# Kernel optimization log

Hardware: AMD Instinct MI355X
Metric: run time of the kernel (lower is better)

The kernel has to match this reference:

```python
import jax, jax.numpy as jnp
import numpy as np

H = 256  # GRU hidden size
V = 56   # decoder vocab / fc1 out


def gru_cell(x, h, wih, whh, bih, bhh):
    # PyTorch GRU cell math (gate order: r, z, n)
    gi = x @ wih.T + bih
    gh = h @ whh.T + bhh
    ir, iz, inn = jnp.split(gi, 3, axis=-1)
    hr, hz, hn = jnp.split(gh, 3, axis=-1)
    r = jax.nn.sigmoid(ir + hr)
    z = jax.nn.sigmoid(iz + hz)
    n = jnp.tanh(inn + r * hn)
    return (1.0 - z) * n + z * h


def gru_scan(seq, h0, wih, whh, bih, bhh):
    def step(h, xt):
        h = gru_cell(xt, h, wih, whh, bih, bhh)
        return h, h
    hT, ys = jax.lax.scan(step, h0, seq)
    return ys, hT


def bigru(seq, pf, pb):
    # seq: (S, N, F). Returns (S, N, 2H), final fwd hidden (N,H), final bwd hidden (N,H)
    S, N, _ = seq.shape
    h0 = jnp.zeros((N, H), seq.dtype)
    yf, hf = gru_scan(seq, h0, *pf)
    yb_rev, hb = gru_scan(seq[::-1], h0, *pb)
    return jnp.concatenate([yf, yb_rev[::-1]], axis=-1), hf, hb


def setup_inputs() -> dict:
    key = jax.random.key(0)
    ks = iter(jax.random.split(key, 32))
    s = 0.05
    p = {}
    p["x"] = jax.random.normal(next(ks), (64, 48, 512, 2, 2), dtype=jnp.float32)
    # bi_gru_1: input 192
    for d in ("f", "b"):
        p[f"w_ih_1{d}"] = jax.random.normal(next(ks), (3 * H, 192), jnp.float32) * s
        p[f"w_hh_1{d}"] = jax.random.normal(next(ks), (3 * H, H), jnp.float32) * s
        p[f"b_ih_1{d}"] = jax.random.normal(next(ks), (3 * H,), jnp.float32) * s
        p[f"b_hh_1{d}"] = jax.random.normal(next(ks), (3 * H,), jnp.float32) * s
    # bi_gru_2: input 512
    for d in ("f", "b"):
        p[f"w_ih_2{d}"] = jax.random.normal(next(ks), (3 * H, 2 * H), jnp.float32) * s
        p[f"w_hh_2{d}"] = jax.random.normal(next(ks), (3 * H, H), jnp.float32) * s
        p[f"b_ih_2{d}"] = jax.random.normal(next(ks), (3 * H,), jnp.float32) * s
        p[f"b_hh_2{d}"] = jax.random.normal(next(ks), (3 * H,), jnp.float32) * s
    # decoder GRU: input 56
    p["w_ih_d"] = jax.random.normal(next(ks), (3 * H, V), jnp.float32) * s
    p["w_hh_d"] = jax.random.normal(next(ks), (3 * H, H), jnp.float32) * s
    p["b_ih_d"] = jax.random.normal(next(ks), (3 * H,), jnp.float32) * s
    p["b_hh_d"] = jax.random.normal(next(ks), (3 * H,), jnp.float32) * s
    p["w_fc1"] = jax.random.normal(next(ks), (V, H), jnp.float32) * s
    p["b_fc1"] = jax.random.normal(next(ks), (V,), jnp.float32) * s
    p["w_adj"] = jax.random.normal(next(ks), (H, 2 * H), jnp.float32) * s
    p["b_adj"] = jax.random.normal(next(ks), (H,), jnp.float32) * s
    p["target_length"] = 6
    return p


def reference(x,
              w_ih_1f, w_hh_1f, b_ih_1f, b_hh_1f,
              w_ih_1b, w_hh_1b, b_ih_1b, b_hh_1b,
              w_ih_2f, w_hh_2f, b_ih_2f, b_hh_2f,
              w_ih_2b, w_hh_2b, b_ih_2b, b_hh_2b,
              w_ih_d, w_hh_d, b_ih_d, b_hh_d,
              w_fc1, b_fc1, w_adj, b_adj,
              target_length):
    B, C, T, Hh, Ww = x.shape
    # permute(2,0,1,3,4).contiguous().view(B, T, -1): flat buffer in (T,B,..) order reshaped to (B,T,feat)
    seq = jnp.transpose(x, (2, 0, 1, 3, 4)).reshape(B, T, C * Hh * Ww)
    # GRUs run seq-first: seq dim = B, batch dim = T (faithful to the torch code)
    y1, _, _ = bigru(seq, (w_ih_1f, w_hh_1f, b_ih_1f, b_hh_1f),
                     (w_ih_1b, w_hh_1b, b_ih_1b, b_hh_1b))
    # dropout is identity at inference
    y2, hf, hb = bigru(y1, (w_ih_2f, w_hh_2f, b_ih_2f, b_hh_2f),
                       (w_ih_2b, w_hh_2b, b_ih_2b, b_hh_2b))
    combined = jnp.concatenate([hf, hb], axis=-1)       # (T, 2H)
    dec_h_all = combined @ w_adj.T + b_adj              # (T, H)
    dec_h = dec_h_all[:B]                               # loop over b in range(B) selects first B rows
    inp0 = jnp.zeros((B, V), x.dtype)

    def step(carry, _):
        inp, h = carry
        h = gru_cell(inp, h, w_ih_d, w_hh_d, b_ih_d, b_hh_d)
        out = h @ w_fc1.T + b_fc1
        return (out, h), out

    _, outs = jax.lax.scan(step, (inp0, dec_h), None, length=target_length)
    return jnp.transpose(outs, (1, 0, 2))  # (B, target_length, V)
```

## Files before the change

### kernel.cpp

```cpp
#include <hip/hip_runtime.h>
#include <hip/hip_fp16.h>
#include <stdint.h>


#define HD 256
#define G3 768
#define NSEQ 64
#define NSTEP 64

typedef _Float16 hvec2 __attribute__((ext_vector_type(2)));
typedef _Float16 f16x8 __attribute__((ext_vector_type(8)));
typedef float f32x4 __attribute__((ext_vector_type(4)));

__device__ __forceinline__ float sigmf(float x) {
    return 1.0f / (1.0f + __expf(-x));
}

#if __has_builtin(__builtin_amdgcn_fdot2)
__device__ __forceinline__ float fdot2u(uint32_t w, uint32_t h, float acc) {
    return __builtin_amdgcn_fdot2(__builtin_bit_cast(hvec2, w),
                                  __builtin_bit_cast(hvec2, h), acc, false);
}
#else
__device__ __forceinline__ float fdot2u(uint32_t w, uint32_t h, float acc) {
    const __half2 wv = __builtin_bit_cast(__half2, w);
    const __half2 hv = __builtin_bit_cast(__half2, h);
    acc += __half2float(wv.x) * __half2float(hv.x);
    acc += __half2float(wv.y) * __half2float(hv.y);
    return acc;
}
#endif

__device__ __forceinline__ uint32_t pkh(float a, float b) {
    uint32_t lo = __half_as_ushort(__float2half_rn(a));
    uint32_t hi = __half_as_ushort(__float2half_rn(b));
    return lo | (hi << 16);
}

#define L16(X) X(0) X(1) X(2) X(3) X(4) X(5) X(6) X(7) \
  X(8) X(9) X(10) X(11) X(12) X(13) X(14) X(15)

#define LRES(i) \
    const uint4 wr##i = wbase[(i) * G3]; \
    const uint4 wz##i = wbase[(i) * G3 + 256]; \
    const uint4 wn##i = wbase[(i) * G3 + 512];

#define DRES(i) { \
    const uint4 hp = *(const uint4*)&hb[hoff + 4 * (i)]; \
    ar0 = fdot2u(wr##i.x, hp.x, ar0); ar1 = fdot2u(wr##i.y, hp.y, ar1); \
    ar0 = fdot2u(wr##i.z, hp.z, ar0); ar1 = fdot2u(wr##i.w, hp.w, ar1); \
    az0 = fdot2u(wz##i.x, hp.x, az0); az1 = fdot2u(wz##i.y, hp.y, az1); \
    az0 = fdot2u(wz##i.z, hp.z, az0); az1 = fdot2u(wz##i.w, hp.w, az1); \
    an0 = fdot2u(wn##i.x, hp.x, an0); an1 = fdot2u(wn##i.y, hp.y, an1); \
    an0 = fdot2u(wn##i.z, hp.z, an0); an1 = fdot2u(wn##i.w, hp.w, an1); }

__global__ __launch_bounds__(256) void pack_whhT(
    const float* __restrict__ w0, const float* __restrict__ w1,
    const float* __restrict__ w2, const float* __restrict__ w3,
    const float* __restrict__ w4,
    uint32_t* __restrict__ o0, uint32_t* __restrict__ o1,
    uint32_t* __restrict__ o2, uint32_t* __restrict__ o3,
    uint32_t* __restrict__ o4)
{
    const float* w; uint32_t* o;
    switch (blockIdx.y) {
        case 0: w = w0; o = o0; break;
        case 1: w = w1; o = o1; break;
        case 2: w = w2; o = o2; break;
        case 3: w = w3; o = o3; break;
        default: w = w4; o = o4; break;
    }
    int idx = blockIdx.x * 256 + threadIdx.x;
    int j = idx >> 5, q = idx & 31;
    const float4 fa = *(const float4*)(w + j * HD + 8 * q);
    const float4 fb = *(const float4*)(w + j * HD + 8 * q + 4);
    uint4 r;
    r.x = pkh(fa.x, fa.y);
    r.y = pkh(fa.z, fa.w);
    r.z = pkh(fb.x, fb.y);
    r.w = pkh(fb.z, fb.w);
    ((uint4*)o)[q * G3 + j] = r;
}

__global__ __launch_bounds__(256) void pack_wih(
    const float* __restrict__ s0, const float* __restrict__ s1,
    const float* __restrict__ s2, const float* __restrict__ s3,
    __half* __restrict__ d0, __half* __restrict__ d1,
    __half* __restrict__ d2, __half* __restrict__ d3)
{
    const float* s; __half* d; int sz;
    switch (blockIdx.y) {
        case 0: s = s0; d = d0; sz = 147456; break;
        case 1: s = s1; d = d1; sz = 147456; break;
        case 2: s = s2; d = d2; sz = 393216; break;
        default: s = s3; d = d3; sz = 393216; break;
    }
    int i4 = blockIdx.x * 256 + threadIdx.x;
    if (i4 * 4 >= sz) return;
    const float4 v = *(const float4*)(s + i4 * 4);
    __half2 lo; lo.x = __float2half_rn(v.x); lo.y = __float2half_rn(v.y);
    __half2 hi; hi.x = __float2half_rn(v.z); hi.y = __float2half_rn(v.w);
    *(__half2*)(d + i4 * 4)     = lo;
    *(__half2*)(d + i4 * 4 + 2) = hi;
}

__global__ __launch_bounds__(256) void prep_small(
    const float* __restrict__ wihd,
    const float* __restrict__ wadj,
    const float* __restrict__ wfc1,
    float* __restrict__ wihdT,
    float* __restrict__ wadjT,
    float* __restrict__ wfc1T)
{
    int idx = blockIdx.x * 256 + threadIdx.x;
    if (idx < 43008) {
        int v = idx / G3, j = idx % G3;
        wihdT[idx] = wihd[j * 56 + v];
    } else if (idx < 43008 + 131072) {
        int i2 = idx - 43008;
        int f = i2 / HD, i = i2 % HD;
        wadjT[i2] = wadj[i * 512 + f];
    } else {
        int i3 = idx - 174080;
        int k = i3 / 56, v = i3 % 56;
        wfc1T[i3] = wfc1[v * HD + k];
    }
}

__global__ __launch_bounds__(256) void gather_seq(
    const float* __restrict__ x, __half* __restrict__ seqg)
{
    int idx = blockIdx.x * 256 + threadIdx.x;
    int f = idx % 192;
    int m = idx / 192;
    int n = m >> 6, s = m & 63;
    seqg[idx] = __float2half(x[n * 98304 + (f >> 2) * 2048 + s * 32 + (f & 3)]);
}

__global__ __launch_bounds__(256) void gemm_mfma(
    const __half* __restrict__ A,
    const __half* __restrict__ B0, const __half* __restrict__ B1,
    const float* __restrict__ bias0, const float* __restrict__ bias1,
    float* __restrict__ C0, float* __restrict__ C1, int K)
{
    const __half* B    = blockIdx.z ? B1 : B0;
    const float*  bias = blockIdx.z ? bias1 : bias0;
    float*        C    = blockIdx.z ? C1 : C0;
    const int m0 = blockIdx.x * 64;
    const int n0 = blockIdx.y * 64;
    const int w  = threadIdx.x >> 6;
    const int l  = threadIdx.x & 63;
    const int lr = l & 15;
    const int lk = (l >> 4) * 8;

    const __half* arow = A + (size_t)(m0 + w * 16 + lr) * K + lk;
    const __half* brow = B + (size_t)(n0 + lr) * K + lk;

    f32x4 acc0 = {0.f, 0.f, 0.f, 0.f};
    f32x4 acc1 = acc0, acc2 = acc0, acc3 = acc0;

#pragma unroll 2
    for (int k0 = 0; k0 < K; k0 += 32) {
        const f16x8 a  = *(const f16x8*)(arow + k0);
        const f16x8 b0 = *(const f16x8*)(brow + k0);
        const f16x8 b1 = *(const f16x8*)(brow + 16 * K + k0);
        const f16x8 b2 = *(const f16x8*)(brow + 32 * K + k0);
        const f16x8 b3 = *(const f16x8*)(brow + 48 * K + k0);
        acc0 = __builtin_amdgcn_mfma_f32_16x16x32_f16(a, b0, acc0, 0, 0, 0);
        acc1 = __builtin_amdgcn_mfma_f32_16x16x32_f16(a, b1, acc1, 0, 0, 0);
        acc2 = __builtin_amdgcn_mfma_f32_16x16x32_f16(a, b2, acc2, 0, 0, 0);
        acc3 = __builtin_amdgcn_mfma_f32_16x16x32_f16(a, b3, acc3, 0, 0, 0);
    }

    const int crow = m0 + w * 16 + (l >> 4) * 4;
    const int ccol = n0 + lr;
    float* cp = C + (size_t)crow * G3 + ccol;
    const float bb0 = bias[ccol];
    const float bb1 = bias[ccol + 16];
    const float bb2 = bias[ccol + 32];
    const float bb3 = bias[ccol + 48];
#pragma unroll
    for (int j = 0; j < 4; ++j) {
        cp[(size_t)j * G3 +  0] = acc0[j] + bb0;
        cp[(size_t)j * G3 + 16] = acc1[j] + bb1;
        cp[(size_t)j * G3 + 32] = acc2[j] + bb2;
        cp[(size_t)j * G3 + 48] = acc3[j] + bb3;
    }
}

__global__ __launch_bounds__(512, 1) void gru_scan(
    const float* __restrict__ giF, const float* __restrict__ giB,
    const uint32_t* __restrict__ wTF, const uint32_t* __restrict__ wTB,
    const float* __restrict__ bhhF, const float* __restrict__ bhhB,
    __half* __restrict__ y1, float* __restrict__ hfin, int mode)
{
    const int dir = blockIdx.x & 1;
    const int n   = blockIdx.x >> 1;
    const int t   = threadIdx.x;
    const int tr  = t & 255;
    const int kh  = t >> 8;
    const int hoff = kh * 64;
    const float* gi  = dir ? giB : giF;
    const float* bhh = dir ? bhhB : bhhF;
    const uint4* wbase = (const uint4*)(dir ? wTB : wTF) + (size_t)(kh * 16) * G3 + tr;

    __shared__ __align__(16) uint32_t h1u[2][HD / 2];
    __shared__ float ph_r[HD], ph_z[HD], ph_n[HD];
    __shared__ float gin[2][G3];

    L16(LRES)
    const float bhr = bhh[tr], bhz = bhh[256 + tr], bhn = bhh[512 + tr];

    const float* gbase = gi + (size_t)n * NSTEP * G3;
    const int s0 = dir ? (NSTEP - 1) : 0;
#pragma unroll
    for (int i = t; i < G3; i += 512) gin[0][i] = gbase[s0 * G3 + i];

    float h_own = 0.0f;
    if (t < HD / 2) h1u[0][t] = 0u;
    __syncthreads();

    int s = s0;
    for (int step = 0; step < NSTEP; ++step) {
        const uint32_t* hb = h1u[step & 1];
        float ar0 = 0.f, ar1 = 0.f;
        float az0 = 0.f, az1 = 0.f;
        float an0 = 0.f, an1 = 0.f;
        L16(DRES)

        if (kh) {
            ph_r[tr] = ar0 + ar1;
            ph_z[tr] = az0 + az1;
            ph_n[tr] = an0 + an1;
        }
        __syncthreads();
        const int s_nxt = dir ? (step < NSTEP - 1 ? NSTEP - 2 - step : 0)
                              : (step < NSTEP - 1 ? step + 1 : NSTEP - 1);
        if (kh == 0) {
            const float* gcur = gin[step & 1];
            const float ghr = (ar0 + ar1) + ph_r[tr] + bhr;
            const float ghz = (az0 + az1) + ph_z[tr] + bhz;
            const float ghn = (an0 + an1) + ph_n[tr] + bhn;
            const float r  = sigmf(gcur[tr] + ghr);
            const float z  = sigmf(gcur[256 + tr] + ghz);
            const float nn = tanhf(gcur[512 + tr] + r * ghn);
            const float hnew = (1.0f - z) * nn + z * h_own;
            h_own = hnew;
            const __half hh = __float2half(hnew);
            ((__half*)h1u[(step + 1) & 1])[tr] = hh;
            if (mode == 0)
                y1[(size_t)(n * NSTEP + s) * 512 + dir * HD + tr] = hh;
        } else {
            float* gnxt = gin[(step + 1) & 1];
#pragma unroll
            for (int i = tr; i < G3; i += 256)
                gnxt[i] = gbase[s_nxt * G3 + i];
        }
        s = s_nxt;
        __syncthreads();
    }
    if (mode == 1 && kh == 0)
        hfin[(size_t)(dir * NSEQ + n) * HD + tr] = h_own;
}

__global__ __launch_bounds__(256) void adj_kernel(
    const float* __restrict__ hfin, const float* __restrict__ wadjT,
    const float* __restrict__ badj, float* __restrict__ dech)
{
    const int n = blockIdx.x, t = threadIdx.x;
    __shared__ float comb[512];
    comb[t]      = hfin[(size_t)n * HD + t];
    comb[HD + t] = hfin[(size_t)(NSEQ + n) * HD + t];
    __syncthreads();
    float acc = badj[t];
#pragma unroll 8
    for (int f = 0; f < 512; ++f) acc += wadjT[f * HD + t] * comb[f];
    dech[n * HD + t] = acc;
}

__global__ __launch_bounds__(768, 3) void decoder_kernel(
    const float* __restrict__ dech, const uint32_t* __restrict__ wTd,
    const float* __restrict__ wihdT, const float* __restrict__ bihd,
    const float* __restrict__ bhhd, const float* __restrict__ wfc1T,
    const float* __restrict__ bfc1, float* __restrict__ out)
{
    const int n = blockIdx.x, t = threadIdx.x;
    const uint4* wq = (const uint4*)wTd + t;

    __shared__ __align__(16) uint32_t h1u[2][HD / 2];
    __shared__ float ghs[G3], gis[G3];
    __shared__ float hfp[HD];
    __shared__ float inp[56];
    __shared__ float pf1[448];

    const float bi = bihd[t], bh = bhhd[t];

    float h_own = 0.0f;
    if (t < HD) {
        const float hv = dech[(size_t)n * HD + t];
        h_own = hv;
        ((__half*)h1u[0])[t] = __float2half(hv);
        hfp[t] = hv;
    }
    if (t < 56) inp[t] = 0.0f;
    __syncthreads();

    for (int step = 0; step < 6; ++step) {
        const uint32_t* hb = h1u[step & 1];
        float a0 = 0.f, a1 = 0.f;
#pragma unroll 8
        for (int q = 0; q < 32; ++q) {
            const uint4 w = wq[q * G3];
            const uint4 hp = *(const uint4*)&hb[4 * q];
            a0 = fdot2u(w.x, hp.x, a0); a1 = fdot2u(w.y, hp.y, a1);
            a0 = fdot2u(w.z, hp.z, a0); a1 = fdot2u(w.w, hp.w, a1);
        }
        float ai = bi;
#pragma unroll 8
        for (int v = 0; v < 56; ++v) ai += wihdT[v * G3 + t] * inp[v];
        ghs[t] = a0 + a1 + bh;
        gis[t] = ai;
        __syncthreads();
        if (t < HD) {
            const float r  = sigmf(gis[t] + ghs[t]);
            const float z  = sigmf(gis[HD + t] + ghs[HD + t]);
            const float nn = tanhf(gis[2 * HD + t] + r * ghs[2 * HD + t]);
            const float hnew = (1.0f - z) * nn + z * h_own;
            h_own = hnew;
            ((__half*)h1u[(step + 1) & 1])[t] = __float2half(hnew);
            hfp[t] = hnew;
        }
        __syncthreads();
        if (t < 448) {
            const int v = t >> 3, g = t & 7;
            float o = 0.f;
#pragma unroll
            for (int k2 = 0; k2 < 32; ++k2)
                o += wfc1T[(g * 32 + k2) * 56 + v] * hfp[g * 32 + k2];
            pf1[t] = o;
        }
        __syncthreads();
        if (t < 56) {
            float o = bfc1[t];
#pragma unroll
            for (int g = 0; g < 8; ++g) o += pf1[t * 8 + g];
            out[(size_t)n * 336 + step * 56 + t] = o;
            inp[t] = o;
        }
        __syncthreads();
    }
}

extern "C" void kernel_launch(void* const* d_in, const int* in_sizes, int n_in,
                              void* d_out, int out_size, void* d_ws, size_t ws_size,
                              hipStream_t stream)
{
    const float* x      = (const float*)d_in[0];
    const float* wih1f  = (const float*)d_in[1];
    const float* whh1f  = (const float*)d_in[2];
    const float* bih1f  = (const float*)d_in[3];
    const float* bhh1f  = (const float*)d_in[4];
    const float* wih1b  = (const float*)d_in[5];
    const float* whh1b  = (const float*)d_in[6];
    const float* bih1b  = (const float*)d_in[7];
    const float* bhh1b  = (const float*)d_in[8];
    const float* wih2f  = (const float*)d_in[9];
    const float* whh2f  = (const float*)d_in[10];
    const float* bih2f  = (const float*)d_in[11];
    const float* bhh2f  = (const float*)d_in[12];
    const float* wih2b  = (const float*)d_in[13];
    const float* whh2b  = (const float*)d_in[14];
    const float* bih2b  = (const float*)d_in[15];
    const float* bhh2b  = (const float*)d_in[16];
    const float* wihd   = (const float*)d_in[17];
    const float* whhd   = (const float*)d_in[18];
    const float* bihd   = (const float*)d_in[19];
    const float* bhhd   = (const float*)d_in[20];
    const float* wfc1   = (const float*)d_in[21];
    const float* bfc1   = (const float*)d_in[22];
    const float* wadj   = (const float*)d_in[23];
    const float* badj   = (const float*)d_in[24];

    float* ws = (float*)d_ws;
    __half*   seqg_h  = (__half*)(ws + 0);
    float*    gi_f    = ws + 393216;
    float*    gi_b    = ws + 3538944;
    __half*   y1h     = (__half*)(ws + 6684672);
    float*    hfin    = ws + 7733248;
    float*    dech    = ws + 7766016;
    uint32_t* wt1f    = (uint32_t*)(ws + 7782400);
    uint32_t* wt1b    = (uint32_t*)(ws + 7880704);
    uint32_t* wt2f    = (uint32_t*)(ws + 7979008);
    uint32_t* wt2b    = (uint32_t*)(ws + 8077312);
    uint32_t* wtd     = (uint32_t*)(ws + 8175616);
    __half*   wih1f_h = (__half*)(ws + 8273920);
    __half*   wih1b_h = (__half*)(ws + 8347648);
    __half*   wih2f_h = (__half*)(ws + 8421376);
    __half*   wih2b_h = (__half*)(ws + 8617984);
    float*    wihdT   = ws + 8814592;
    float*    wadjT   = ws + 8857600;
    float*    wfc1T   = ws + 8988672;

    pack_whhT<<<dim3(96, 5), 256, 0, stream>>>(
        whh1f, whh1b, whh2f, whh2b, whhd, wt1f, wt1b, wt2f, wt2b, wtd);
    pack_wih<<<dim3(384, 4), 256, 0, stream>>>(
        wih1f, wih1b, wih2f, wih2b, wih1f_h, wih1b_h, wih2f_h, wih2b_h);
    prep_small<<<736, 256, 0, stream>>>(wihd, wadj, wfc1, wihdT, wadjT, wfc1T);
    gather_seq<<<3072, 256, 0, stream>>>(x, seqg_h);

    gemm_mfma<<<dim3(64, 12, 2), 256, 0, stream>>>(
        seqg_h, wih1f_h, wih1b_h, bih1f, bih1b, gi_f, gi_b, 192);
    gru_scan<<<128, 512, 0, stream>>>(
        gi_f, gi_b, wt1f, wt1b, bhh1f, bhh1b, y1h, hfin, 0);

    gemm_mfma<<<dim3(64, 12, 2), 256, 0, stream>>>(
        y1h, wih2f_h, wih2b_h, bih2f, bih2b, gi_f, gi_b, 512);
    gru_scan<<<128, 512, 0, stream>>>(
        gi_f, gi_b, wt2f, wt2b, bhh2f, bhh2b, y1h, hfin, 1);

    adj_kernel<<<64, 256, 0, stream>>>(hfin, wadjT, badj, dech);
    decoder_kernel<<<64, 768, 0, stream>>>(
        dech, wtd, wihdT, bihd, bhhd, wfc1T, bfc1, (float*)d_out);
}
```

Measured before the change: 353.2 us.

## Restructure GRU scan to one thread per gate row with 768 threads

The recurrent GRU scan kernel now uses 768 threads, one per gate output row, each holding the full 256-wide fp16 weight row in registers. This replaces 512 threads that split K in half and combined partial sums through shared memory. Input-gate values are prefetched per thread from global memory instead of double-buffered in shared memory, and the y1 output is written as packed 32-bit words after a second barrier. This raises parallelism and removes the partial-sum exchange, at the cost of an extra barrier per step, more register pressure (32 uint4 per thread), and y1 now also being written in the second layer where it was previously skipped.

```diff
diff --git a/kernel.cpp b/kernel.cpp
--- a/kernel.cpp
+++ b/kernel.cpp
@@ -37,22 +37,15 @@
     return lo | (hi << 16);
 }
 
-#define L16(X) X(0) X(1) X(2) X(3) X(4) X(5) X(6) X(7) \
-  X(8) X(9) X(10) X(11) X(12) X(13) X(14) X(15)
-
-#define LRES(i) \
-    const uint4 wr##i = wbase[(i) * G3]; \
-    const uint4 wz##i = wbase[(i) * G3 + 256]; \
-    const uint4 wn##i = wbase[(i) * G3 + 512];
-
-#define DRES(i) { \
-    const uint4 hp = *(const uint4*)&hb[hoff + 4 * (i)]; \
-    ar0 = fdot2u(wr##i.x, hp.x, ar0); ar1 = fdot2u(wr##i.y, hp.y, ar1); \
-    ar0 = fdot2u(wr##i.z, hp.z, ar0); ar1 = fdot2u(wr##i.w, hp.w, ar1); \
-    az0 = fdot2u(wz##i.x, hp.x, az0); az1 = fdot2u(wz##i.y, hp.y, az1); \
-    az0 = fdot2u(wz##i.z, hp.z, az0); az1 = fdot2u(wz##i.w, hp.w, az1); \
-    an0 = fdot2u(wn##i.x, hp.x, an0); an1 = fdot2u(wn##i.y, hp.y, an1); \
-    an0 = fdot2u(wn##i.z, hp.z, an0); an1 = fdot2u(wn##i.w, hp.w, an1); }
+#define L32(X) X(0) X(1) X(2) X(3) X(4) X(5) X(6) X(7) \
+  X(8) X(9) X(10) X(11) X(12) X(13) X(14) X(15) \
+  X(16) X(17) X(18) X(19) X(20) X(21) X(22) X(23) \
+  X(24) X(25) X(26) X(27) X(28) X(29) X(30) X(31)
+
+#define LWG(i) const uint4 w##i = wq[(i) * G3];
+#define DWG(i) { const uint4 hp = *(const uint4*)&hb[4 * (i)]; \
+    a0 = fdot2u(w##i.x, hp.x, a0); a1 = fdot2u(w##i.y, hp.y, a1); \
+    a2 = fdot2u(w##i.z, hp.z, a2); a3 = fdot2u(w##i.w, hp.w, a3); }
 
 __global__ __launch_bounds__(256) void pack_whhT(
     const float* __restrict__ w0, const float* __restrict__ w1,
@@ -188,79 +181,68 @@
     }
 }
 
-__global__ __launch_bounds__(512, 1) void gru_scan(
-    const float* __restrict__ giF, const float* __restrict__ giB,
-    const uint32_t* __restrict__ wTF, const uint32_t* __restrict__ wTB,
+__global__ __launch_bounds__(768, 3) void gru_scan(
+    const float* giF, const float* giB,
+    const uint32_t* wTF, const uint32_t* wTB,
     const float* __restrict__ bhhF, const float* __restrict__ bhhB,
-    __half* __restrict__ y1, float* __restrict__ hfin, int mode)
+    uint32_t* y1u, float* hfin)
 {
     const int dir = blockIdx.x & 1;
     const int n   = blockIdx.x >> 1;
     const int t   = threadIdx.x;
-    const int tr  = t & 255;
-    const int kh  = t >> 8;
-    const int hoff = kh * 64;
     const float* gi  = dir ? giB : giF;
     const float* bhh = dir ? bhhB : bhhF;
-    const uint4* wbase = (const uint4*)(dir ? wTB : wTF) + (size_t)(kh * 16) * G3 + tr;
+    const uint4* wq  = (const uint4*)(dir ? wTB : wTF) + t;
 
     __shared__ __align__(16) uint32_t h1u[2][HD / 2];
-    __shared__ float ph_r[HD], ph_z[HD], ph_n[HD];
-    __shared__ float gin[2][G3];
-
-    L16(LRES)
-    const float bhr = bhh[tr], bhz = bhh[256 + tr], bhn = bhh[512 + tr];
-
-    const float* gbase = gi + (size_t)n * NSTEP * G3;
-    const int s0 = dir ? (NSTEP - 1) : 0;
-#pragma unroll
-    for (int i = t; i < G3; i += 512) gin[0][i] = gbase[s0 * G3 + i];
+    __shared__ float s_rz[2 * HD];
+    __shared__ float s_ghn[HD], s_inn[HD];
+
+    L32(LWG)
+    const float bh = bhh[t];
 
     float h_own = 0.0f;
     if (t < HD / 2) h1u[0][t] = 0u;
     __syncthreads();
 
-    int s = s0;
+    const float* gbase = gi + (size_t)n * NSTEP * G3;
+    int s = dir ? (NSTEP - 1) : 0;
+    float g_own = gbase[s * G3 + t];
+
     for (int step = 0; step < NSTEP; ++step) {
-        const uint32_t* hb = h1u[step & 1];
-        float ar0 = 0.f, ar1 = 0.f;
-        float az0 = 0.f, az1 = 0.f;
-        float an0 = 0.f, an1 = 0.f;
-        L16(DRES)
-
-        if (kh) {
-            ph_r[tr] = ar0 + ar1;
-            ph_z[tr] = az0 + az1;
-            ph_n[tr] = an0 + an1;
-        }
-        __syncthreads();
         const int s_nxt = dir ? (step < NSTEP - 1 ? NSTEP - 2 - step : 0)
                               : (step < NSTEP - 1 ? step + 1 : NSTEP - 1);
-        if (kh == 0) {
-            const float* gcur = gin[step & 1];
-            const float ghr = (ar0 + ar1) + ph_r[tr] + bhr;
-            const float ghz = (az0 + az1) + ph_z[tr] + bhz;
-            const float ghn = (an0 + an1) + ph_n[tr] + bhn;
-            const float r  = sigmf(gcur[tr] + ghr);
-            const float z  = sigmf(gcur[256 + tr] + ghz);
-            const float nn = tanhf(gcur[512 + tr] + r * ghn);
+        const float g_nxt = gbase[s_nxt * G3 + t];
+
+        const uint32_t* hb = h1u[step & 1];
+        float a0 = 0.f, a1 = 0.f, a2 = 0.f, a3 = 0.f;
+        L32(DWG)
+        const float acc = bh + ((a0 + a1) + (a2 + a3));
+
+        if (t < 2 * HD) {
+            s_rz[t] = g_own + acc;
+        } else {
+            s_ghn[t - 2 * HD] = acc;
+            s_inn[t - 2 * HD] = g_own;
+        }
+        __syncthreads();
+        if (t < HD) {
+            const float r  = sigmf(s_rz[t]);
+            const float z  = sigmf(s_rz[HD + t]);
+            const float nn = tanhf(s_inn[t] + r * s_ghn[t]);
             const float hnew = (1.0f - z) * nn + z * h_own;
             h_own = hnew;
-            const __half hh = __float2half(hnew);
-            ((__half*)h1u[(step + 1) & 1])[tr] = hh;
-            if (mode == 0)
-                y1[(size_t)(n * NSTEP + s) * 512 + dir * HD + tr] = hh;
-        } else {
-            float* gnxt = gin[(step + 1) & 1];
-#pragma unroll
-            for (int i = tr; i < G3; i += 256)
-                gnxt[i] = gbase[s_nxt * G3 + i];
-        }
+            ((__half*)h1u[(step + 1) & 1])[t] = __float2half(hnew);
+        }
+        __syncthreads();
+        if (t < HD / 2)
+            y1u[(size_t)(n * NSTEP + s) * 256 + dir * 128 + t] =
+                h1u[(step + 1) & 1][t];
+        g_own = g_nxt;
         s = s_nxt;
-        __syncthreads();
-    }
-    if (mode == 1 && kh == 0)
-        hfin[(size_t)(dir * NSEQ + n) * HD + tr] = h_own;
+    }
+    if (t < HD)
+        hfin[(size_t)(dir * NSEQ + n) * HD + t] = h_own;
 }
 
 __global__ __launch_bounds__(256) void adj_kernel(
@@ -385,7 +367,7 @@
     __half*   seqg_h  = (__half*)(ws + 0);
     float*    gi_f    = ws + 393216;
     float*    gi_b    = ws + 3538944;
-    __half*   y1h     = (__half*)(ws + 6684672);
+    uint32_t* y1u     = (uint32_t*)(ws + 6684672);
     float*    hfin    = ws + 7733248;
     float*    dech    = ws + 7766016;
     uint32_t* wt1f    = (uint32_t*)(ws + 7782400);
@@ -410,13 +392,13 @@
 
     gemm_mfma<<<dim3(64, 12, 2), 256, 0, stream>>>(
         seqg_h, wih1f_h, wih1b_h, bih1f, bih1b, gi_f, gi_b, 192);
-    gru_scan<<<128, 512, 0, stream>>>(
-        gi_f, gi_b, wt1f, wt1b, bhh1f, bhh1b, y1h, hfin, 0);
+    gru_scan<<<128, 768, 0, stream>>>(
+        gi_f, gi_b, wt1f, wt1b, bhh1f, bhh1b, y1u, hfin);
 
     gemm_mfma<<<dim3(64, 12, 2), 256, 0, stream>>>(
-        y1h, wih2f_h, wih2b_h, bih2f, bih2b, gi_f, gi_b, 512);
-    gru_scan<<<128, 512, 0, stream>>>(
-        gi_f, gi_b, wt2f, wt2b, bhh2f, bhh2b, y1h, hfin, 1);
+        (const __half*)y1u, wih2f_h, wih2b_h, bih2f, bih2b, gi_f, gi_b, 512);
+    gru_scan<<<128, 768, 0, stream>>>(
+        gi_f, gi_b, wt2f, wt2b, bhh2f, bhh2b, y1u, hfin);
 
     adj_kernel<<<64, 256, 0, stream>>>(hfin, wadjT, badj, dech);
     decoder_kernel<<<64, 768, 0, stream>>>(
```

Result: slower. 366.7 us (+3.8%).

## Batch two sequences per GRU scan block and fuse prep kernels

Applied to the files above, without the earlier changes.

The GRU scan kernel now handles two batch sequences per block. Both thread halves compute partial recurrent dot products for both sequences, and the recurrent weights are streamed from global memory each step instead of being held in registers. This halves the grid and lets each weight load serve two sequences, but adds per-step global/L2 load latency on the serial critical path. The input-gate values are now prefetched into registers rather than staged through shared memory. Separately, the four weight-packing and gather kernels are merged into one launch to cut launch overhead.

```diff
diff --git a/kernel.cpp b/kernel.cpp
--- a/kernel.cpp
+++ b/kernel.cpp
@@ -37,104 +37,77 @@
     return lo | (hi << 16);
 }
 
-#define L16(X) X(0) X(1) X(2) X(3) X(4) X(5) X(6) X(7) \
-  X(8) X(9) X(10) X(11) X(12) X(13) X(14) X(15)
-
-#define LRES(i) \
-    const uint4 wr##i = wbase[(i) * G3]; \
-    const uint4 wz##i = wbase[(i) * G3 + 256]; \
-    const uint4 wn##i = wbase[(i) * G3 + 512];
-
-#define DRES(i) { \
-    const uint4 hp = *(const uint4*)&hb[hoff + 4 * (i)]; \
-    ar0 = fdot2u(wr##i.x, hp.x, ar0); ar1 = fdot2u(wr##i.y, hp.y, ar1); \
-    ar0 = fdot2u(wr##i.z, hp.z, ar0); ar1 = fdot2u(wr##i.w, hp.w, ar1); \
-    az0 = fdot2u(wz##i.x, hp.x, az0); az1 = fdot2u(wz##i.y, hp.y, az1); \
-    az0 = fdot2u(wz##i.z, hp.z, az0); az1 = fdot2u(wz##i.w, hp.w, az1); \
-    an0 = fdot2u(wn##i.x, hp.x, an0); an1 = fdot2u(wn##i.y, hp.y, an1); \
-    an0 = fdot2u(wn##i.z, hp.z, an0); an1 = fdot2u(wn##i.w, hp.w, an1); }
-
-__global__ __launch_bounds__(256) void pack_whhT(
-    const float* __restrict__ w0, const float* __restrict__ w1,
-    const float* __restrict__ w2, const float* __restrict__ w3,
-    const float* __restrict__ w4,
-    uint32_t* __restrict__ o0, uint32_t* __restrict__ o1,
-    uint32_t* __restrict__ o2, uint32_t* __restrict__ o3,
-    uint32_t* __restrict__ o4)
-{
-    const float* w; uint32_t* o;
-    switch (blockIdx.y) {
-        case 0: w = w0; o = o0; break;
-        case 1: w = w1; o = o1; break;
-        case 2: w = w2; o = o2; break;
-        case 3: w = w3; o = o3; break;
-        default: w = w4; o = o4; break;
-    }
-    int idx = blockIdx.x * 256 + threadIdx.x;
-    int j = idx >> 5, q = idx & 31;
-    const float4 fa = *(const float4*)(w + j * HD + 8 * q);
-    const float4 fb = *(const float4*)(w + j * HD + 8 * q + 4);
-    uint4 r;
-    r.x = pkh(fa.x, fa.y);
-    r.y = pkh(fa.z, fa.w);
-    r.z = pkh(fb.x, fb.y);
-    r.w = pkh(fb.z, fb.w);
-    ((uint4*)o)[q * G3 + j] = r;
-}
-
-__global__ __launch_bounds__(256) void pack_wih(
-    const float* __restrict__ s0, const float* __restrict__ s1,
-    const float* __restrict__ s2, const float* __restrict__ s3,
-    __half* __restrict__ d0, __half* __restrict__ d1,
-    __half* __restrict__ d2, __half* __restrict__ d3)
-{
-    const float* s; __half* d; int sz;
-    switch (blockIdx.y) {
-        case 0: s = s0; d = d0; sz = 147456; break;
-        case 1: s = s1; d = d1; sz = 147456; break;
-        case 2: s = s2; d = d2; sz = 393216; break;
-        default: s = s3; d = d3; sz = 393216; break;
-    }
-    int i4 = blockIdx.x * 256 + threadIdx.x;
-    if (i4 * 4 >= sz) return;
-    const float4 v = *(const float4*)(s + i4 * 4);
-    __half2 lo; lo.x = __float2half_rn(v.x); lo.y = __float2half_rn(v.y);
-    __half2 hi; hi.x = __float2half_rn(v.z); hi.y = __float2half_rn(v.w);
-    *(__half2*)(d + i4 * 4)     = lo;
-    *(__half2*)(d + i4 * 4 + 2) = hi;
-}
-
-__global__ __launch_bounds__(256) void prep_small(
-    const float* __restrict__ wihd,
-    const float* __restrict__ wadj,
+__global__ __launch_bounds__(256) void prep_all(
+    const float* __restrict__ whh1f, const float* __restrict__ whh1b,
+    const float* __restrict__ whh2f, const float* __restrict__ whh2b,
+    const float* __restrict__ whhd,
+    uint32_t* __restrict__ wt1f, uint32_t* __restrict__ wt1b,
+    uint32_t* __restrict__ wt2f, uint32_t* __restrict__ wt2b,
+    uint32_t* __restrict__ wtd,
+    const float* __restrict__ wih1f, const float* __restrict__ wih1b,
+    const float* __restrict__ wih2f, const float* __restrict__ wih2b,
+    __half* __restrict__ wih1f_h, __half* __restrict__ wih1b_h,
+    __half* __restrict__ wih2f_h, __half* __restrict__ wih2b_h,
+    const float* __restrict__ wihd, const float* __restrict__ wadj,
     const float* __restrict__ wfc1,
-    float* __restrict__ wihdT,
-    float* __restrict__ wadjT,
-    float* __restrict__ wfc1T)
-{
-    int idx = blockIdx.x * 256 + threadIdx.x;
-    if (idx < 43008) {
-        int v = idx / G3, j = idx % G3;
-        wihdT[idx] = wihd[j * 56 + v];
-    } else if (idx < 43008 + 131072) {
-        int i2 = idx - 43008;
-        int f = i2 / HD, i = i2 % HD;
-        wadjT[i2] = wadj[i * 512 + f];
+    float* __restrict__ wihdT, float* __restrict__ wadjT,
+    float* __restrict__ wfc1T,
+    const float* __restrict__ x, __half* __restrict__ seqg)
+{
+    const int b   = blockIdx.x;
+    const int tid = threadIdx.x;
+
+    if (b < 480) {
+        const int y = b / 96;
+        const float* w; uint32_t* o;
+        switch (y) {
+            case 0: w = whh1f; o = wt1f; break;
+            case 1: w = whh1b; o = wt1b; break;
+            case 2: w = whh2f; o = wt2f; break;
+            case 3: w = whh2b; o = wt2b; break;
+            default: w = whhd; o = wtd; break;
+        }
+        const int idx = (b % 96) * 256 + tid;
+        const int j = idx >> 5, q = idx & 31;
+        const float4 fa = *(const float4*)(w + j * HD + 8 * q);
+        const float4 fb = *(const float4*)(w + j * HD + 8 * q + 4);
+        uint4 r;
+        r.x = pkh(fa.x, fa.y); r.y = pkh(fa.z, fa.w);
+        r.z = pkh(fb.x, fb.y); r.w = pkh(fb.z, fb.w);
+        ((uint4*)o)[q * G3 + j] = r;
+    } else if (b < 1536) {
+        const float* s; __half* d; int i4;
+        if (b < 624)       { s = wih1f; d = wih1f_h; i4 = (b - 480) * 256 + tid; }
+        else if (b < 768)  { s = wih1b; d = wih1b_h; i4 = (b - 624) * 256 + tid; }
+        else if (b < 1152) { s = wih2f; d = wih2f_h; i4 = (b - 768) * 256 + tid; }
+        else               { s = wih2b; d = wih2b_h; i4 = (b - 1152) * 256 + tid; }
+        const float4 v = *(const float4*)(s + (size_t)i4 * 4);
+        __half2 lo; lo.x = __float2half_rn(v.x); lo.y = __float2half_rn(v.y);
+        __half2 hi; hi.x = __float2half_rn(v.z); hi.y = __float2half_rn(v.w);
+        *(__half2*)(d + (size_t)i4 * 4)     = lo;
+        *(__half2*)(d + (size_t)i4 * 4 + 2) = hi;
+    } else if (b < 2272) {
+        const int idx = (b - 1536) * 256 + tid;
+        if (idx < 43008) {
+            int v = idx / G3, j = idx % G3;
+            wihdT[idx] = wihd[j * 56 + v];
+        } else if (idx < 43008 + 131072) {
+            int i2 = idx - 43008;
+            int f = i2 / HD, i = i2 % HD;
+            wadjT[i2] = wadj[i * 512 + f];
+        } else {
+            int i3 = idx - 174080;
+            int k = i3 / 56, v = i3 % 56;
+            wfc1T[i3] = wfc1[v * HD + k];
+        }
     } else {
-        int i3 = idx - 174080;
-        int k = i3 / 56, v = i3 % 56;
-        wfc1T[i3] = wfc1[v * HD + k];
-    }
-}
-
-__global__ __launch_bounds__(256) void gather_seq(
-    const float* __restrict__ x, __half* __restrict__ seqg)
-{
-    int idx = blockIdx.x * 256 + threadIdx.x;
-    int f = idx % 192;
-    int m = idx / 192;
-    int n = m >> 6, s = m & 63;
-    seqg[idx] = __float2half(x[n * 98304 + (f >> 2) * 2048 + s * 32 + (f & 3)]);
+        const int idx = (b - 2272) * 256 + tid;
+        const int f = idx % 192;
+        const int m = idx / 192;
+        const int n = m >> 6, s = m & 63;
+        seqg[idx] = __float2half(
+            x[n * 98304 + (f >> 2) * 2048 + s * 32 + (f & 3)]);
+    }
 }
 
 __global__ __launch_bounds__(256) void gemm_mfma(
@@ -192,75 +165,101 @@
     const float* __restrict__ giF, const float* __restrict__ giB,
     const uint32_t* __restrict__ wTF, const uint32_t* __restrict__ wTB,
     const float* __restrict__ bhhF, const float* __restrict__ bhhB,
-    __half* __restrict__ y1, float* __restrict__ hfin, int mode)
+    __half* __restrict__ y1h, float* __restrict__ hfin)
 {
     const int dir = blockIdx.x & 1;
-    const int n   = blockIdx.x >> 1;
+    const int np  = blockIdx.x >> 1;
     const int t   = threadIdx.x;
     const int tr  = t & 255;
     const int kh  = t >> 8;
     const int hoff = kh * 64;
     const float* gi  = dir ? giB : giF;
     const float* bhh = dir ? bhhB : bhhF;
-    const uint4* wbase = (const uint4*)(dir ? wTB : wTF) + (size_t)(kh * 16) * G3 + tr;
-
-    __shared__ __align__(16) uint32_t h1u[2][HD / 2];
-    __shared__ float ph_r[HD], ph_z[HD], ph_n[HD];
-    __shared__ float gin[2][G3];
-
-    L16(LRES)
+    const uint4* wq  = (const uint4*)(dir ? wTB : wTF) + (size_t)(kh * 16) * G3;
+
+    __shared__ __align__(16) uint32_t hA[2][HD / 2], hB[2][HD / 2];
+    __shared__ float phA_r[HD], phA_z[HD], phA_n[HD];
+    __shared__ float phB_r[HD], phB_z[HD], phB_n[HD];
+
     const float bhr = bhh[tr], bhz = bhh[256 + tr], bhn = bhh[512 + tr];
 
-    const float* gbase = gi + (size_t)n * NSTEP * G3;
-    const int s0 = dir ? (NSTEP - 1) : 0;
-#pragma unroll
-    for (int i = t; i < G3; i += 512) gin[0][i] = gbase[s0 * G3 + i];
-
+    const int n_mine = np * 2 + kh;
+    const float* gb_mine = gi + (size_t)n_mine * NSTEP * G3;
+
+    if (t < HD / 2) { hA[0][t] = 0u; hB[0][t] = 0u; }
+    __syncthreads();
+
+    int s = dir ? (NSTEP - 1) : 0;
+    float g_r = gb_mine[s * G3 + tr];
+    float g_z = gb_mine[s * G3 + 256 + tr];
+    float g_n = gb_mine[s * G3 + 512 + tr];
     float h_own = 0.0f;
-    if (t < HD / 2) h1u[0][t] = 0u;
-    __syncthreads();
-
-    int s = s0;
+
     for (int step = 0; step < NSTEP; ++step) {
-        const uint32_t* hb = h1u[step & 1];
-        float ar0 = 0.f, ar1 = 0.f;
-        float az0 = 0.f, az1 = 0.f;
-        float an0 = 0.f, an1 = 0.f;
-        L16(DRES)
-
-        if (kh) {
-            ph_r[tr] = ar0 + ar1;
-            ph_z[tr] = az0 + az1;
-            ph_n[tr] = an0 + an1;
-        }
-        __syncthreads();
         const int s_nxt = dir ? (step < NSTEP - 1 ? NSTEP - 2 - step : 0)
                               : (step < NSTEP - 1 ? step + 1 : NSTEP - 1);
+        const float gn_r = gb_mine[s_nxt * G3 + tr];
+        const float gn_z = gb_mine[s_nxt * G3 + 256 + tr];
+        const float gn_n = gb_mine[s_nxt * G3 + 512 + tr];
+
+        const uint32_t* ha = hA[step & 1];
+        const uint32_t* hb = hB[step & 1];
+        float arA0 = 0.f, arA1 = 0.f, azA0 = 0.f, azA1 = 0.f;
+        float anA0 = 0.f, anA1 = 0.f;
+        float arB0 = 0.f, arB1 = 0.f, azB0 = 0.f, azB1 = 0.f;
+        float anB0 = 0.f, anB1 = 0.f;
+#pragma unroll
+        for (int i = 0; i < 16; ++i) {
+            const uint4 wr_ = wq[i * G3 + tr];
+            const uint4 wz_ = wq[i * G3 + 256 + tr];
+            const uint4 wn_ = wq[i * G3 + 512 + tr];
+            const uint4 pA = *(const uint4*)&ha[hoff + 4 * i];
+            const uint4 pB = *(const uint4*)&hb[hoff + 4 * i];
+            arA0 = fdot2u(wr_.x, pA.x, arA0); arA1 = fdot2u(wr_.y, pA.y, arA1);
+            arA0 = fdot2u(wr_.z, pA.z, arA0); arA1 = fdot2u(wr_.w, pA.w, arA1);
+            azA0 = fdot2u(wz_.x, pA.x, azA0); azA1 = fdot2u(wz_.y, pA.y, azA1);
+            azA0 = fdot2u(wz_.z, pA.z, azA0); azA1 = fdot2u(wz_.w, pA.w, azA1);
+            anA0 = fdot2u(wn_.x, pA.x, anA0); anA1 = fdot2u(wn_.y, pA.y, anA1);
+            anA0 = fdot2u(wn_.z, pA.z, anA0); anA1 = fdot2u(wn_.w, pA.w, anA1);
+            arB0 = fdot2u(wr_.x, pB.x, arB0); arB1 = fdot2u(wr_.y, pB.y, arB1);
+            arB0 = fdot2u(wr_.z, pB.z, arB0); arB1 = fdot2u(wr_.w, pB.w, arB1);
+            azB0 = fdot2u(wz_.x, pB.x, azB0); azB1 = fdot2u(wz_.y, pB.y, azB1);
+            azB0 = fdot2u(wz_.z, pB.z, azB0); azB1 = fdot2u(wz_.w, pB.w, azB1);
+            anB0 = fdot2u(wn_.x, pB.x, anB0); anB1 = fdot2u(wn_.y, pB.y, anB1);
+            anB0 = fdot2u(wn_.z, pB.z, anB0); anB1 = fdot2u(wn_.w, pB.w, anB1);
+        }
         if (kh == 0) {
-            const float* gcur = gin[step & 1];
-            const float ghr = (ar0 + ar1) + ph_r[tr] + bhr;
-            const float ghz = (az0 + az1) + ph_z[tr] + bhz;
-            const float ghn = (an0 + an1) + ph_n[tr] + bhn;
-            const float r  = sigmf(gcur[tr] + ghr);
-            const float z  = sigmf(gcur[256 + tr] + ghz);
-            const float nn = tanhf(gcur[512 + tr] + r * ghn);
+            phB_r[tr] = arB0 + arB1;
+            phB_z[tr] = azB0 + azB1;
+            phB_n[tr] = anB0 + anB1;
+        } else {
+            phA_r[tr] = arA0 + arA1;
+            phA_z[tr] = azA0 + azA1;
+            phA_n[tr] = anA0 + anA1;
+        }
+        __syncthreads();
+        {
+            const float mr = kh ? (arB0 + arB1) + phB_r[tr]
+                                : (arA0 + arA1) + phA_r[tr];
+            const float mz = kh ? (azB0 + azB1) + phB_z[tr]
+                                : (azA0 + azA1) + phA_z[tr];
+            const float mn = kh ? (anB0 + anB1) + phB_n[tr]
+                                : (anA0 + anA1) + phA_n[tr];
+            const float r  = sigmf(g_r + mr + bhr);
+            const float z  = sigmf(g_z + mz + bhz);
+            const float nn = tanhf(g_n + r * (mn + bhn));
             const float hnew = (1.0f - z) * nn + z * h_own;
             h_own = hnew;
-            const __half hh = __float2half(hnew);
-            ((__half*)h1u[(step + 1) & 1])[tr] = hh;
-            if (mode == 0)
-                y1[(size_t)(n * NSTEP + s) * 512 + dir * HD + tr] = hh;
-        } else {
-            float* gnxt = gin[(step + 1) & 1];
-#pragma unroll
-            for (int i = tr; i < G3; i += 256)
-                gnxt[i] = gbase[s_nxt * G3 + i];
-        }
+            uint32_t* hnx = kh ? hB[(step + 1) & 1] : hA[(step + 1) & 1];
+            ((__half*)hnx)[tr] = __float2half(hnew);
+            y1h[(size_t)(n_mine * NSTEP + s) * 512 + dir * HD + tr] =
+                __float2half(hnew);
+        }
+        g_r = gn_r; g_z = gn_z; g_n = gn_n;
         s = s_nxt;
         __syncthreads();
     }
-    if (mode == 1 && kh == 0)
-        hfin[(size_t)(dir * NSEQ + n) * HD + tr] = h_own;
+    hfin[(size_t)(dir * NSEQ + n_mine) * HD + tr] = h_own;
 }
 
 __global__ __launch_bounds__(256) void adj_kernel(
@@ -401,22 +400,23 @@
     float*    wadjT   = ws + 8857600;
     float*    wfc1T   = ws + 8988672;
 
-    pack_whhT<<<dim3(96, 5), 256, 0, stream>>>(
-        whh1f, whh1b, whh2f, whh2b, whhd, wt1f, wt1b, wt2f, wt2b, wtd);
-    pack_wih<<<dim3(384, 4), 256, 0, stream>>>(
-        wih1f, wih1b, wih2f, wih2b, wih1f_h, wih1b_h, wih2f_h, wih2b_h);
-    prep_small<<<736, 256, 0, stream>>>(wihd, wadj, wfc1, wihdT, wadjT, wfc1T);
-    gather_seq<<<3072, 256, 0, stream>>>(x, seqg_h);
+    prep_all<<<5344, 256, 0, stream>>>(
+        whh1f, whh1b, whh2f, whh2b, whhd,
+        wt1f, wt1b, wt2f, wt2b, wtd,
+        wih1f, wih1b, wih2f, wih2b,
+        wih1f_h, wih1b_h, wih2f_h, wih2b_h,
+        wihd, wadj, wfc1, wihdT, wadjT, wfc1T,
+        x, seqg_h);
 
     gemm_mfma<<<dim3(64, 12, 2), 256, 0, stream>>>(
         seqg_h, wih1f_h, wih1b_h, bih1f, bih1b, gi_f, gi_b, 192);
-    gru_scan<<<128, 512, 0, stream>>>(
-        gi_f, gi_b, wt1f, wt1b, bhh1f, bhh1b, y1h, hfin, 0);
+    gru_scan<<<64, 512, 0, stream>>>(
+        gi_f, gi_b, wt1f, wt1b, bhh1f, bhh1b, y1h, hfin);
 
     gemm_mfma<<<dim3(64, 12, 2), 256, 0, stream>>>(
         y1h, wih2f_h, wih2b_h, bih2f, bih2b, gi_f, gi_b, 512);
-    gru_scan<<<128, 512, 0, stream>>>(
-        gi_f, gi_b, wt2f, wt2b, bhh2f, bhh2b, y1h, hfin, 1);
+    gru_scan<<<64, 512, 0, stream>>>(
+        gi_f, gi_b, wt2f, wt2b, bhh2f, bhh2b, y1h, hfin);
 
     adj_kernel<<<64, 256, 0, stream>>>(hfin, wadjT, badj, dech);
     decoder_kernel<<<64, 768, 0, stream>>>(
```

Result: slower. 838.4 us (+137.4%).
